# Kernel optimization log

Hardware: AMD Instinct MI355X
Metric: run time of the kernel (lower is better)

## Reference

```python
import jax, jax.numpy as jnp
import numpy as np
import math

B, S, D, H = 4, 2048, 2048, 16
HD = D // H  # 128


def _alibi_slopes(n_heads):
    # standard ALiBi slopes: 2^(-8/n * (h+1))
    return jnp.asarray([2.0 ** (-8.0 / n_heads * (h + 1)) for h in range(n_heads)], dtype=jnp.float32)


def setup_inputs() -> dict:
    key = jax.random.key(0)
    ks = jax.random.split(key, 10)
    w = lambda k: jax.random.normal(k, (D, D), dtype=jnp.float32) * 0.02
    b = lambda k: jax.random.normal(k, (D,), dtype=jnp.float32) * 0.01
    return {
        "hidden_states": jax.random.normal(ks[0], (B, S, D), dtype=jnp.float32),
        "Wq": w(ks[1]), "bq": b(ks[2]),
        "Wk": w(ks[3]), "bk": b(ks[4]),
        "Wv": w(ks[5]), "bv": b(ks[6]),
        "Wo": w(ks[7]), "bo": b(ks[8]),
        "alibi_slopes": _alibi_slopes(H),
    }


def reference(hidden_states, Wq, bq, Wk, bk, Wv, bv, Wo, bo, alibi_slopes):
    Bn, t, _ = hidden_states.shape
    split = lambda x: x.reshape(Bn, t, H, HD).transpose(0, 2, 1, 3)  # [B,H,S,hd]
    q = split(hidden_states @ Wq.T + bq)
    k = split(hidden_states @ Wk.T + bk)
    v = split(hidden_states @ Wv.T + bv)

    scores = jnp.einsum("bhsd,bhtd->bhst", q, k)  # [B,H,S,S]
    pos = jnp.arange(t)
    # alibi bias added BEFORE the 1/sqrt(hd) scaling, as in the torch code
    rel = (pos[None, :] - pos[:, None]).astype(scores.dtype)  # j - i
    bias = alibi_slopes[:, None, None] * rel  # [H,S,S]
    scores = (scores + bias[None]) / math.sqrt(HD)
    # grok-style tanh rescaling
    scores = 30.0 * jnp.tanh(scores / 30.0)
    causal = pos[:, None] >= pos[None, :]  # [S,S]
    scores = jnp.where(causal[None, None], scores, -jnp.inf)
    probs = jax.nn.softmax(scores, axis=-1)
    ctx = jnp.einsum("bhst,bhtd->bhsd", probs, v)
    ctx = ctx.transpose(0, 2, 1, 3).reshape(Bn, t, D)
    return ctx @ Wo.T + bo
```

## Files before the change

### kernel.cpp

```cpp
#include <hip/hip_runtime.h>

typedef unsigned int u32;
typedef unsigned short u16;
typedef __bf16 bf16x8 __attribute__((ext_vector_type(8)));
typedef float f32x4 __attribute__((ext_vector_type(4)));
typedef float f32x2 __attribute__((ext_vector_type(2)));


__device__ __forceinline__ u16 f2bf(float f) {
  u32 u = __builtin_bit_cast(u32, f);
  u32 r = u + 0x7fffu + ((u >> 16) & 1u);
  return (u16)(r >> 16);
}

__device__ __forceinline__ u32 cvtpk_bf16(float a, float b) {
  u32 d;
  asm("v_cvt_pk_bf16_f32 %0, %1, %2" : "=v"(d) : "v"(a), "v"(b));
  return d;
}

__device__ __forceinline__ void gload_lds16(const void* g, void* l) {
  __builtin_amdgcn_global_load_lds(
      (__attribute__((address_space(1))) void*)(g),
      (__attribute__((address_space(3))) void*)(l), 16, 0, 0);
}


__global__ __launch_bounds__(256) void convert_kernel(
    const float* __restrict__ hs, const float* __restrict__ wq,
    const float* __restrict__ wk, const float* __restrict__ wv,
    const float* __restrict__ wo,
    u16* __restrict__ hsb, u16* __restrict__ wqb, u16* __restrict__ wkb,
    u16* __restrict__ wvb, u16* __restrict__ wob) {
  long t = (long)blockIdx.x * 256 + threadIdx.x;
  const float* src;
  u16* dst;
  long off;
  if (t < 2097152) {
    src = hs; dst = hsb; off = t << 3;
  } else {
    long u = t - 2097152;
    int wi = (int)(u >> 19);
    off = (u & 524287) << 3;
    if (wi == 0)      { src = wq; dst = wqb; }
    else if (wi == 1) { src = wk; dst = wkb; }
    else if (wi == 2) { src = wv; dst = wvb; }
    else              { src = wo; dst = wob; }
  }
  float4 a = *(const float4*)(src + off);
  float4 b = *(const float4*)(src + off + 4);
  uint4 o;
  o.x = (u32)f2bf(a.x) | ((u32)f2bf(a.y) << 16);
  o.y = (u32)f2bf(a.z) | ((u32)f2bf(a.w) << 16);
  o.z = (u32)f2bf(b.x) | ((u32)f2bf(b.y) << 16);
  o.w = (u32)f2bf(b.z) | ((u32)f2bf(b.w) << 16);
  *(uint4*)(dst + off) = o;
}


template <int OF32>
__global__ __launch_bounds__(512, 2) void gemm256_kernel(
    const u16* __restrict__ A, const u16* __restrict__ Bw,
    const float* __restrict__ bias0, const float* __restrict__ bias1,
    const float* __restrict__ bias2, void* __restrict__ o0,
    void* __restrict__ o1, void* __restrict__ o2, int m_tiles, int n_tiles) {
  __shared__ __align__(16) char L[2][2][2][16384];

  const int tid = threadIdx.x;
  const int lane = tid & 63, w = tid >> 6;
  const int lr = lane & 15, lk = lane >> 4;
  const int wm = (w >> 2) * 128, wn = (w & 3) * 64;

  const int bid = blockIdx.x;
  const int xcd = bid & 7, loc = bid >> 3;
  const int npx = n_tiles >> 3;
  const int n_idx = xcd * npx + loc % npx;
  const int m_idx = loc / npx;
  const int m0 = m_idx * 256, n0 = n_idx * 256;

  const char* Ab = (const char*)A;
  const char* Bb = (const char*)Bw;
  const char* gA[2];
  const char* gB[2];
#pragma unroll
  for (int j = 0; j < 2; j++) {
    const int o = j * 8192 + tid * 16;
    const int row = o >> 6;
    const int c = (o & 63) ^ (((row >> 1) & 3) << 4);
    gA[j] = Ab + (size_t)(m0 + row) * 4096 + c;
    gB[j] = Bb + (size_t)(n0 + row) * 4096 + c;
  }

  auto stage = [&](int t, int kh, int isB) {
    char* Ld = &L[t & 1][isB][kh][0] + tid * 16;
    const int gof = t * 128 + kh * 64;
#pragma unroll
    for (int j = 0; j < 2; j++)
      gload_lds16((isB ? gB[j] : gA[j]) + gof, Ld + j * 8192);
  };
  auto rdA = [&](bf16x8* dst, int buf, int kh, int mset) {
#pragma unroll
    for (int m = 0; m < 4; m++) {
      const int row = wm + mset * 64 + m * 16 + lr;
      const int c = (lk * 16) ^ (((row >> 1) & 3) << 4);
      dst[m] = *(const bf16x8*)(&L[buf][0][kh][0] + row * 64 + c);
    }
  };
  auto rdB = [&](bf16x8* dst, int buf, int kh) {
#pragma unroll
    for (int n = 0; n < 4; n++) {
      const int row = wn + n * 16 + lr;
      const int c = (lk * 16) ^ (((row >> 1) & 3) << 4);
      dst[n] = *(const bf16x8*)(&L[buf][1][kh][0] + row * 64 + c);
    }
  };

  f32x4 acc[2][4][4];
#pragma unroll
  for (int s = 0; s < 2; s++)
#pragma unroll
    for (int m = 0; m < 4; m++)
#pragma unroll
      for (int n = 0; n < 4; n++) acc[s][m][n] = {0.f, 0.f, 0.f, 0.f};

  auto mm = [&](f32x4 (&ac)[4][4], bf16x8* a_, bf16x8* b_) {
    __builtin_amdgcn_s_setprio(1);
#pragma unroll
    for (int m = 0; m < 4; m++)
#pragma unroll
      for (int n = 0; n < 4; n++)
        ac[m][n] = __builtin_amdgcn_mfma_f32_16x16x32_bf16(a_[m], b_[n],
                                                           ac[m][n], 0, 0, 0);
    __builtin_amdgcn_s_setprio(0);
  };

  stage(0, 0, 0); stage(0, 0, 1); stage(0, 1, 0); stage(0, 1, 1);

  bf16x8 aP[4], aQ[4], b0[4], b1[4];
  for (int t = 0; t < 32; ++t) {
    const int buf = t & 1;
    const int t1 = (t + 1 < 32) ? t + 1 : 31;
    asm volatile("s_waitcnt vmcnt(4)" ::: "memory");
    asm volatile("s_barrier" ::: "memory");
    rdA(aP, buf, 0, 0);
    rdB(b0, buf, 0);
    stage(t1, 0, 0);
    if (t) mm(acc[1], aQ, b1);
    rdA(aQ, buf, 0, 1);
    stage(t1, 0, 1);
    mm(acc[0], aP, b0);
    asm volatile("s_waitcnt vmcnt(4)" ::: "memory");
    asm volatile("s_barrier" ::: "memory");
    rdA(aP, buf, 1, 0);
    rdB(b1, buf, 1);
    stage(t1, 1, 0);
    mm(acc[1], aQ, b0);
    rdA(aQ, buf, 1, 1);
    stage(t1, 1, 1);
    mm(acc[0], aP, b1);
  }
  mm(acc[1], aQ, b1);

  const float* bias;
  void* op;
  int nl0;
  if (OF32) {
    bias = bias0; op = o0; nl0 = n0;
  } else {
    const int seg = n0 >> 11;
    bias = seg == 0 ? bias0 : (seg == 1 ? bias1 : bias2);
    op = seg == 0 ? o0 : (seg == 1 ? o1 : o2);
    nl0 = n0 & 2047;
  }
#pragma unroll
  for (int n = 0; n < 4; n++) {
    const int col = nl0 + wn + n * 16 + lr;
    const float bv = bias[col];
#pragma unroll
    for (int s = 0; s < 2; s++)
#pragma unroll
      for (int m = 0; m < 4; m++) {
        const int grow = m0 + wm + s * 64 + m * 16 + lk * 4;
#pragma unroll
        for (int r = 0; r < 4; r++) {
          const float v = acc[s][m][n][r] + bv;
          if (OF32)
            ((float*)op)[(size_t)(grow + r) * 2048 + col] = v;
          else
            ((u16*)op)[(size_t)(grow + r) * 2048 + col] = f2bf(v);
        }
      }
  }
}


__global__ __launch_bounds__(512, 2) void attn_kernel(
    const u16* __restrict__ Qm, const u16* __restrict__ Km,
    const u16* __restrict__ Vm, const float* __restrict__ slopes,
    u16* __restrict__ ctx) {
  __shared__ __align__(16) char Ks[2][64 * 256];
  __shared__ __align__(16) char Vt[128 * 128];
  __shared__ __align__(16) char Pb[8][16 * 128];

  const int bid = blockIdx.x;
  const int sw = (bid & 7) * 64 + (bid >> 3);
  const int bh = sw >> 3, pi = sw & 7;
  const int b = bh >> 4, h = bh & 15;
  const int NTA = 2 * pi + 2;

  const int tid = threadIdx.x;
  const int lane = tid & 63, w = tid >> 6;
  const int lr = lane & 15, lk = lane >> 4;

  const char* Qb = (const char*)Qm + (size_t)b * 2048 * 4096 + h * 256;
  const char* Kb = (const char*)Km + (size_t)b * 2048 * 4096 + h * 256;
  const char* Vb = (const char*)Vm + (size_t)b * 2048 * 4096 + h * 256;

  const float SCALE = 0.08838834764831845f;
  const float sl_c = slopes[h] * SCALE;

  const f32x2 C1v = {1.4426950408889634f, 1.4426950408889634f};
  const f32x2 C3v = {-5.343315e-4f, -5.343315e-4f};
  const f32x2 C5v = {2.374806e-7f, 2.374806e-7f};
  const f32x2 C7v = {-1.068005e-10f, -1.068005e-10f};
  const f32x2 SC2 = {SCALE, SCALE};
  const f32x2 NEG16 = {-16.0f, -16.0f};
  const f32x2 POS16 = {16.0f, 16.0f};

  f32x2 zo2[8];
#pragma unroll
  for (int nb = 0; nb < 4; nb++)
#pragma unroll
    for (int p = 0; p < 2; p++) {
      zo2[nb * 2 + p][0] = sl_c * (float)((lr - lk * 4) + nb * 16 - (2 * p));
      zo2[nb * 2 + p][1] = sl_c * (float)((lr - lk * 4) + nb * 16 - (2 * p + 1));
    }

  const int vd0 = (tid & 15) * 8;
  const int vkv2 = tid >> 4;

  uint4 vr0, vr1;

  auto kvt_of = [&](int it) { return it < NTA ? it : it - NTA; };

  auto stageK = [&](int it, int buf) {
    const int kv0 = kvt_of(it) * 64;
#pragma unroll
    for (int j = 0; j < 2; j++) {
      const int o = j * 8192 + tid * 16;
      const int row = o >> 8, c = (o & 255) ^ ((row & 7) << 4);
      gload_lds16(Kb + (size_t)(kv0 + row) * 4096 + c, Ks[buf] + o);
    }
  };
  auto loadV = [&](int it) {
    const int kv0 = kvt_of(it) * 64;
    vr0 = *(const uint4*)(Vb + (size_t)(kv0 + vkv2 * 2) * 4096 + vd0 * 2);
    vr1 = *(const uint4*)(Vb + (size_t)(kv0 + vkv2 * 2 + 1) * 4096 + vd0 * 2);
  };
  auto writeV = [&]() {
    const u32* p0 = (const u32*)&vr0;
    const u32* p1 = (const u32*)&vr1;
#pragma unroll
    for (int wd = 0; wd < 4; wd++) {
      const u32 ev = __builtin_amdgcn_perm(p1[wd], p0[wd], 0x05040100u);
      const u32 od = __builtin_amdgcn_perm(p1[wd], p0[wd], 0x07060302u);
      const int d0_ = vd0 + 2 * wd, d1_ = d0_ + 1;
      *(u32*)(Vt + d0_ * 128 +
              ((vkv2 * 4) ^ (((d0_ ^ (d0_ >> 3)) & 7) << 4))) = ev;
      *(u32*)(Vt + d1_ * 128 +
              ((vkv2 * 4) ^ (((d1_ ^ (d1_ >> 3)) & 7) << 4))) = od;
    }
  };

  bf16x8 qf[4];
  f32x4 pv[8];
  f32x2 rs2[2];
  int q0 = 0;

  stageK(0, 0);
  loadV(0);

  for (int it = 0; it < 34; ++it) {
    const int kb = it & 1;
    const int kv0 = kvt_of(it) * 64;

    if (it == 0 || it == NTA) {
      const int st = (it == 0) ? pi : (15 - pi);
      q0 = st * 128 + w * 16;
#pragma unroll
      for (int kc = 0; kc < 4; kc++)
        qf[kc] =
            *(const bf16x8*)(Qb + (size_t)(q0 + lr) * 4096 + kc * 64 + lk * 16);
#pragma unroll
      for (int i = 0; i < 8; i++) pv[i] = {0.f, 0.f, 0.f, 0.f};
      rs2[0] = {0.f, 0.f};
      rs2[1] = {0.f, 0.f};
    }

    __syncthreads();
    writeV();
    asm volatile("s_waitcnt vmcnt(0)" ::: "memory");
    __syncthreads();

    if (it + 1 < 34) {
      stageK(it + 1, kb ^ 1);
      loadV(it + 1);
    }

    f32x4 sc[4];
    __builtin_amdgcn_s_setprio(1);
#pragma unroll
    for (int nb = 0; nb < 4; nb++) {
      f32x4 a = {0.f, 0.f, 0.f, 0.f};
      const int krow = nb * 16 + lr;
#pragma unroll
      for (int kc = 0; kc < 4; kc++) {
        const int off = krow * 256 + ((kc * 64 + lk * 16) ^ ((krow & 7) << 4));
        bf16x8 kf = *(const bf16x8*)(Ks[kb] + off);
        a = __builtin_amdgcn_mfma_f32_16x16x32_bf16(qf[kc], kf, a, 0, 0, 0);
      }
      sc[nb] = a;
    }
    __builtin_amdgcn_s_setprio(0);

    const bool diag = (it < NTA) ? (it >= NTA - 2) : (it >= 32);
    const float sb = sl_c * (float)(kv0 - q0);
    const f32x2 sb2 = {sb, sb};
#pragma unroll
    for (int nb = 0; nb < 4; nb++) {
#pragma unroll
      for (int p = 0; p < 2; p++) {
        f32x2 s2 = {sc[nb][2 * p], sc[nb][2 * p + 1]};
        f32x2 z = __builtin_elementwise_fma(s2, SC2, zo2[nb * 2 + p] + sb2);
        z = __builtin_elementwise_max(z, NEG16);
        z = __builtin_elementwise_min(z, POS16);
        const f32x2 u2 = z * z;
        f32x2 hh = __builtin_elementwise_fma(u2, C7v, C5v);
        hh = __builtin_elementwise_fma(u2, hh, C3v);
        hh = __builtin_elementwise_fma(u2, hh, C1v);
        const f32x2 ee = z * hh;
        float p0 = exp2f(ee[0]);
        float p1 = exp2f(ee[1]);
        if (diag) {
          const int kv = kv0 + nb * 16 + lr;
          const int qA = q0 + lk * 4 + 2 * p;
          p0 = (kv <= qA) ? p0 : 0.0f;
          p1 = (kv <= qA + 1) ? p1 : 0.0f;
        }
        f32x2 pr = {p0, p1};
        rs2[p] += pr;
        const u32 pk = cvtpk_bf16(p0, p1);
        const int qq0 = lk * 4 + 2 * p;
        const int qq1 = qq0 + 1;
        const int off0 = qq0 * 128 + (((nb * 16 + lr) * 2) ^ ((qq0 & 7) << 4));
        const int off1 = qq1 * 128 + (((nb * 16 + lr) * 2) ^ ((qq1 & 7) << 4));
        *(u16*)(Pb[w] + off0) = (u16)pk;
        *(u16*)(Pb[w] + off1) = (u16)(pk >> 16);
      }
    }

    __builtin_amdgcn_s_setprio(1);
#pragma unroll
    for (int kc = 0; kc < 2; kc++) {
      const int poff = lr * 128 + ((kc * 64 + lk * 16) ^ ((lr & 7) << 4));
      bf16x8 pf = *(const bf16x8*)(Pb[w] + poff);
#pragma unroll
      for (int db = 0; db < 8; db++) {
        const int d = db * 16 + lr;
        const int voff =
            d * 128 + ((kc * 64 + lk * 16) ^ (((d ^ (d >> 3)) & 7) << 4));
        bf16x8 vf = *(const bf16x8*)(Vt + voff);
        pv[db] = __builtin_amdgcn_mfma_f32_16x16x32_bf16(pf, vf, pv[db], 0, 0, 0);
      }
    }
    __builtin_amdgcn_s_setprio(0);

    if (it == NTA - 1 || it == 33) {
      float inv[4];
#pragma unroll
      for (int r = 0; r < 4; r++) {
        float s = (r < 2) ? rs2[0][r & 1] : rs2[1][r & 1];
        s += __shfl_xor(s, 1);
        s += __shfl_xor(s, 2);
        s += __shfl_xor(s, 4);
        s += __shfl_xor(s, 8);
        inv[r] = 1.0f / s;
      }
      const size_t baserow = (size_t)b * 2048 + q0 + lk * 4;
#pragma unroll
      for (int db = 0; db < 8; db++)
#pragma unroll
        for (int r = 0; r < 4; r++)
          ctx[(baserow + r) * 2048 + h * 128 + db * 16 + lr] =
              f2bf(pv[db][r] * inv[r]);
    }
  }
}


extern "C" void kernel_launch(void* const* d_in, const int* in_sizes, int n_in,
                              void* d_out, int out_size, void* d_ws,
                              size_t ws_size, hipStream_t stream) {
  const float* hs = (const float*)d_in[0];
  const float* Wq = (const float*)d_in[1];
  const float* bq = (const float*)d_in[2];
  const float* Wk = (const float*)d_in[3];
  const float* bk = (const float*)d_in[4];
  const float* Wv = (const float*)d_in[5];
  const float* bv = (const float*)d_in[6];
  const float* Wo = (const float*)d_in[7];
  const float* bo = (const float*)d_in[8];
  const float* slopes = (const float*)d_in[9];

  char* ws = (char*)d_ws;
  u16* hsb = (u16*)(ws);
  u16* wqb = (u16*)(ws + 33554432);
  u16* wkb = (u16*)(ws + 41943040);
  u16* wvb = (u16*)(ws + 50331648);
  u16* wob = (u16*)(ws + 58720256);
  u16* Qb  = (u16*)(ws + 67108864);
  u16* Kb  = (u16*)(ws + 100663296);
  u16* Vb  = (u16*)(ws + 134217728);
  u16* ctxb = hsb;

  convert_kernel<<<16384, 256, 0, stream>>>(hs, Wq, Wk, Wv, Wo, hsb, wqb, wkb,
                                            wvb, wob);
  gemm256_kernel<0><<<768, 512, 0, stream>>>(hsb, wqb, bq, bk, bv, Qb, Kb, Vb,
                                             32, 24);
  attn_kernel<<<512, 512, 0, stream>>>(Qb, Kb, Vb, slopes, ctxb);
  gemm256_kernel<1><<<256, 512, 0, stream>>>(ctxb, wob, bo, bo, bo, d_out,
                                             d_out, d_out, 32, 8);
}
```

Before: 472.8 us.

## Double attention query tile per warp to 32 rows and halve the grid

Each warp now processes two 16-row query sub-tiles, so each block covers 256 query rows instead of 128, and the grid shrinks from 512 to 256 blocks. The aim is to reuse each K and V tile loaded into shared memory across twice as many queries, cutting LDS and global traffic per unit of MFMA work. The cost is roughly double the accumulator and Q-fragment registers, a larger P buffer in LDS, and fewer blocks to spread across the GPU's compute units, which may leave some units idle and lower occupancy under the existing launch bounds.

```diff
diff --git a/kernel.cpp b/kernel.cpp
--- a/kernel.cpp
+++ b/kernel.cpp
@@ -200,13 +200,13 @@
     u16* __restrict__ ctx) {
   __shared__ __align__(16) char Ks[2][64 * 256];
   __shared__ __align__(16) char Vt[128 * 128];
-  __shared__ __align__(16) char Pb[8][16 * 128];
+  __shared__ __align__(16) char Pb[8][32 * 128];
 
   const int bid = blockIdx.x;
-  const int sw = (bid & 7) * 64 + (bid >> 3);
-  const int bh = sw >> 3, pi = sw & 7;
+  const int sw = (bid & 7) * 32 + (bid >> 3);
+  const int bh = sw >> 2, pi = sw & 3;
   const int b = bh >> 4, h = bh & 15;
-  const int NTA = 2 * pi + 2;
+  const int NTA = 4 * pi + 4;
 
   const int tid = threadIdx.x;
   const int lane = tid & 63, w = tid >> 6;
@@ -272,29 +272,34 @@
     }
   };
 
-  bf16x8 qf[4];
-  f32x4 pv[8];
-  f32x2 rs2[2];
+  bf16x8 qf[2][4];
+  f32x4 pv[2][8];
+  f32x2 rs2[2][2];
   int q0 = 0;
 
   stageK(0, 0);
   loadV(0);
 
-  for (int it = 0; it < 34; ++it) {
+  for (int it = 0; it < 36; ++it) {
     const int kb = it & 1;
     const int kv0 = kvt_of(it) * 64;
 
     if (it == 0 || it == NTA) {
-      const int st = (it == 0) ? pi : (15 - pi);
-      q0 = st * 128 + w * 16;
-#pragma unroll
-      for (int kc = 0; kc < 4; kc++)
-        qf[kc] =
-            *(const bf16x8*)(Qb + (size_t)(q0 + lr) * 4096 + kc * 64 + lk * 16);
-#pragma unroll
-      for (int i = 0; i < 8; i++) pv[i] = {0.f, 0.f, 0.f, 0.f};
-      rs2[0] = {0.f, 0.f};
-      rs2[1] = {0.f, 0.f};
+      const int st = (it == 0) ? pi : (7 - pi);
+      q0 = st * 256 + w * 32;
+#pragma unroll
+      for (int mi = 0; mi < 2; mi++)
+#pragma unroll
+        for (int kc = 0; kc < 4; kc++)
+          qf[mi][kc] = *(const bf16x8*)(Qb + (size_t)(q0 + mi * 16 + lr) * 4096 +
+                                        kc * 64 + lk * 16);
+#pragma unroll
+      for (int mi = 0; mi < 2; mi++) {
+#pragma unroll
+        for (int i = 0; i < 8; i++) pv[mi][i] = {0.f, 0.f, 0.f, 0.f};
+        rs2[mi][0] = {0.f, 0.f};
+        rs2[mi][1] = {0.f, 0.f};
+      }
     }
 
     __syncthreads();
@@ -302,97 +307,123 @@
     asm volatile("s_waitcnt vmcnt(0)" ::: "memory");
     __syncthreads();
 
-    if (it + 1 < 34) {
+    if (it + 1 < 36) {
       stageK(it + 1, kb ^ 1);
       loadV(it + 1);
     }
 
-    f32x4 sc[4];
+    f32x4 sc[2][4];
     __builtin_amdgcn_s_setprio(1);
 #pragma unroll
     for (int nb = 0; nb < 4; nb++) {
-      f32x4 a = {0.f, 0.f, 0.f, 0.f};
       const int krow = nb * 16 + lr;
+      bf16x8 kf[4];
 #pragma unroll
       for (int kc = 0; kc < 4; kc++) {
         const int off = krow * 256 + ((kc * 64 + lk * 16) ^ ((krow & 7) << 4));
-        bf16x8 kf = *(const bf16x8*)(Ks[kb] + off);
-        a = __builtin_amdgcn_mfma_f32_16x16x32_bf16(qf[kc], kf, a, 0, 0, 0);
-      }
-      sc[nb] = a;
+        kf[kc] = *(const bf16x8*)(Ks[kb] + off);
+      }
+#pragma unroll
+      for (int mi = 0; mi < 2; mi++) {
+        f32x4 a = {0.f, 0.f, 0.f, 0.f};
+#pragma unroll
+        for (int kc = 0; kc < 4; kc++)
+          a = __builtin_amdgcn_mfma_f32_16x16x32_bf16(qf[mi][kc], kf[kc], a, 0,
+                                                      0, 0);
+        sc[mi][nb] = a;
+      }
     }
     __builtin_amdgcn_s_setprio(0);
 
-    const bool diag = (it < NTA) ? (it >= NTA - 2) : (it >= 32);
+    const bool diag = (it < NTA) ? (it >= NTA - 4) : (it >= 32);
     const float sb = sl_c * (float)(kv0 - q0);
-    const f32x2 sb2 = {sb, sb};
-#pragma unroll
-    for (int nb = 0; nb < 4; nb++) {
-#pragma unroll
-      for (int p = 0; p < 2; p++) {
-        f32x2 s2 = {sc[nb][2 * p], sc[nb][2 * p + 1]};
-        f32x2 z = __builtin_elementwise_fma(s2, SC2, zo2[nb * 2 + p] + sb2);
-        z = __builtin_elementwise_max(z, NEG16);
-        z = __builtin_elementwise_min(z, POS16);
-        const f32x2 u2 = z * z;
-        f32x2 hh = __builtin_elementwise_fma(u2, C7v, C5v);
-        hh = __builtin_elementwise_fma(u2, hh, C3v);
-        hh = __builtin_elementwise_fma(u2, hh, C1v);
-        const f32x2 ee = z * hh;
-        float p0 = exp2f(ee[0]);
-        float p1 = exp2f(ee[1]);
-        if (diag) {
-          const int kv = kv0 + nb * 16 + lr;
-          const int qA = q0 + lk * 4 + 2 * p;
-          p0 = (kv <= qA) ? p0 : 0.0f;
-          p1 = (kv <= qA + 1) ? p1 : 0.0f;
+#pragma unroll
+    for (int mi = 0; mi < 2; mi++) {
+      const float sbm = sb - sl_c * (float)(16 * mi);
+      const f32x2 sb2 = {sbm, sbm};
+#pragma unroll
+      for (int nb = 0; nb < 4; nb++) {
+#pragma unroll
+        for (int p = 0; p < 2; p++) {
+          f32x2 s2 = {sc[mi][nb][2 * p], sc[mi][nb][2 * p + 1]};
+          f32x2 z = __builtin_elementwise_fma(s2, SC2, zo2[nb * 2 + p] + sb2);
+          z = __builtin_elementwise_max(z, NEG16);
+          z = __builtin_elementwise_min(z, POS16);
+          const f32x2 u2 = z * z;
+          f32x2 hh = __builtin_elementwise_fma(u2, C7v, C5v);
+          hh = __builtin_elementwise_fma(u2, hh, C3v);
+          hh = __builtin_elementwise_fma(u2, hh, C1v);
+          const f32x2 ee = z * hh;
+          float p0 = exp2f(ee[0]);
+          float p1 = exp2f(ee[1]);
+          if (diag) {
+            const int kv = kv0 + nb * 16 + lr;
+            const int qA = q0 + mi * 16 + lk * 4 + 2 * p;
+            p0 = (kv <= qA) ? p0 : 0.0f;
+            p1 = (kv <= qA + 1) ? p1 : 0.0f;
+          }
+          f32x2 pr = {p0, p1};
+          rs2[mi][p] += pr;
+          const u32 pk = cvtpk_bf16(p0, p1);
+          const int qq0 = mi * 16 + lk * 4 + 2 * p;
+          const int qq1 = qq0 + 1;
+          const int off0 =
+              qq0 * 128 + (((nb * 16 + lr) * 2) ^ ((qq0 & 7) << 4));
+          const int off1 =
+              qq1 * 128 + (((nb * 16 + lr) * 2) ^ ((qq1 & 7) << 4));
+          *(u16*)(Pb[w] + off0) = (u16)pk;
+          *(u16*)(Pb[w] + off1) = (u16)(pk >> 16);
         }
-        f32x2 pr = {p0, p1};
-        rs2[p] += pr;
-        const u32 pk = cvtpk_bf16(p0, p1);
-        const int qq0 = lk * 4 + 2 * p;
-        const int qq1 = qq0 + 1;
-        const int off0 = qq0 * 128 + (((nb * 16 + lr) * 2) ^ ((qq0 & 7) << 4));
-        const int off1 = qq1 * 128 + (((nb * 16 + lr) * 2) ^ ((qq1 & 7) << 4));
-        *(u16*)(Pb[w] + off0) = (u16)pk;
-        *(u16*)(Pb[w] + off1) = (u16)(pk >> 16);
       }
     }
 
     __builtin_amdgcn_s_setprio(1);
 #pragma unroll
     for (int kc = 0; kc < 2; kc++) {
-      const int poff = lr * 128 + ((kc * 64 + lk * 16) ^ ((lr & 7) << 4));
-      bf16x8 pf = *(const bf16x8*)(Pb[w] + poff);
+      bf16x8 pf[2];
+#pragma unroll
+      for (int mi = 0; mi < 2; mi++) {
+        const int prow = mi * 16 + lr;
+        const int poff =
+            prow * 128 + ((kc * 64 + lk * 16) ^ ((lr & 7) << 4));
+        pf[mi] = *(const bf16x8*)(Pb[w] + poff);
+      }
 #pragma unroll
       for (int db = 0; db < 8; db++) {
         const int d = db * 16 + lr;
         const int voff =
             d * 128 + ((kc * 64 + lk * 16) ^ (((d ^ (d >> 3)) & 7) << 4));
         bf16x8 vf = *(const bf16x8*)(Vt + voff);
-        pv[db] = __builtin_amdgcn_mfma_f32_16x16x32_bf16(pf, vf, pv[db], 0, 0, 0);
+#pragma unroll
+        for (int mi = 0; mi < 2; mi++)
+          pv[mi][db] = __builtin_amdgcn_mfma_f32_16x16x32_bf16(pf[mi], vf,
+                                                               pv[mi][db], 0,
+                                                               0, 0);
       }
     }
     __builtin_amdgcn_s_setprio(0);
 
-    if (it == NTA - 1 || it == 33) {
-      float inv[4];
-#pragma unroll
-      for (int r = 0; r < 4; r++) {
-        float s = (r < 2) ? rs2[0][r & 1] : rs2[1][r & 1];
-        s += __shfl_xor(s, 1);
-        s += __shfl_xor(s, 2);
-        s += __shfl_xor(s, 4);
-        s += __shfl_xor(s, 8);
-        inv[r] = 1.0f / s;
-      }
-      const size_t baserow = (size_t)b * 2048 + q0 + lk * 4;
-#pragma unroll
-      for (int db = 0; db < 8; db++)
-#pragma unroll
-        for (int r = 0; r < 4; r++)
-          ctx[(baserow + r) * 2048 + h * 128 + db * 16 + lr] =
-              f2bf(pv[db][r] * inv[r]);
+    if (it == NTA - 1 || it == 35) {
+#pragma unroll
+      for (int mi = 0; mi < 2; mi++) {
+        float inv[4];
+#pragma unroll
+        for (int r = 0; r < 4; r++) {
+          float s = (r < 2) ? rs2[mi][0][r & 1] : rs2[mi][1][r & 1];
+          s += __shfl_xor(s, 1);
+          s += __shfl_xor(s, 2);
+          s += __shfl_xor(s, 4);
+          s += __shfl_xor(s, 8);
+          inv[r] = 1.0f / s;
+        }
+        const size_t baserow = (size_t)b * 2048 + q0 + mi * 16 + lk * 4;
+#pragma unroll
+        for (int db = 0; db < 8; db++)
+#pragma unroll
+          for (int r = 0; r < 4; r++)
+            ctx[(baserow + r) * 2048 + h * 128 + db * 16 + lr] =
+                f2bf(pv[mi][db][r] * inv[r]);
+      }
     }
   }
 }
@@ -427,7 +458,7 @@
                                             wvb, wob);
   gemm256_kernel<0><<<768, 512, 0, stream>>>(hsb, wqb, bq, bk, bv, Qb, Kb, Vb,
                                              32, 24);
-  attn_kernel<<<512, 512, 0, stream>>>(Qb, Kb, Vb, slopes, ctxb);
+  attn_kernel<<<256, 512, 0, stream>>>(Qb, Kb, Vb, slopes, ctxb);
   gemm256_kernel<1><<<256, 512, 0, stream>>>(ctxb, wob, bo, bo, bo, d_out,
                                              d_out, d_out, 32, 8);
 }
```

After: 449.7 us, median of 2. -4.9%, faster.
